# Kernel optimization log

Hardware: AMD Instinct MI355X
Metric: run time of the kernel (lower is better)

The kernel has to match this reference:

```python
import jax, jax.numpy as jnp
import numpy as np

N, A, OBS, H, E, ITERS = 2000, 16, 64, 128, 16000, 8


def _init_linear(key, din, dout):
    kw, kb = jax.random.split(key)
    s = 1.0 / np.sqrt(din)
    W = jax.random.uniform(kw, (dout, din), minval=-s, maxval=s, dtype=jnp.float32)
    b = jax.random.uniform(kb, (dout,), minval=-s, maxval=s, dtype=jnp.float32)
    return W, b


def setup_inputs() -> dict:
    key = jax.random.key(0)
    ks = jax.random.split(key, 20)
    x = jax.random.normal(ks[0], (N, OBS), dtype=jnp.float32)
    prev_action = jax.random.normal(ks[1], (N, A), dtype=jnp.float32)
    state = jax.random.normal(ks[2], (1, N, H), dtype=jnp.float32)
    # edges: unique-ish random pairs with i < j (no self loops)
    rng = np.random.default_rng(0)
    ei = rng.integers(0, N - 1, size=E)
    ej = rng.integers(ei + 1, N)
    edges = jnp.asarray(np.stack([ei, ej], axis=1), dtype=jnp.int32)
    # GRU params (torch layout: rows = [r; z; n])
    s = 1.0 / np.sqrt(H)
    gru_wih = jax.random.uniform(ks[3], (3 * H, OBS + A), minval=-s, maxval=s, dtype=jnp.float32)
    gru_whh = jax.random.uniform(ks[4], (3 * H, H), minval=-s, maxval=s, dtype=jnp.float32)
    gru_bih = jax.random.uniform(ks[5], (3 * H,), minval=-s, maxval=s, dtype=jnp.float32)
    gru_bhh = jax.random.uniform(ks[6], (3 * H,), minval=-s, maxval=s, dtype=jnp.float32)
    # utility MLP: [H, 256, 256, A]
    uW0, ub0 = _init_linear(ks[7], H, 256)
    uW1, ub1 = _init_linear(ks[8], 256, 256)
    uW2, ub2 = _init_linear(ks[9], 256, A)
    # payoff MLP: [2H, H, 256, 256, A, A*A]  (faithful to source's dim-list reuse)
    pW0, pb0 = _init_linear(ks[10], 2 * H, H)
    pW1, pb1 = _init_linear(ks[11], H, 256)
    pW2, pb2 = _init_linear(ks[12], 256, 256)
    pW3, pb3 = _init_linear(ks[13], 256, A)
    pW4, pb4 = _init_linear(ks[14], A, A * A)
    return dict(x=x, prev_action=prev_action, state=state, edges=edges,
                gru_wih=gru_wih, gru_whh=gru_whh, gru_bih=gru_bih, gru_bhh=gru_bhh,
                uW0=uW0, ub0=ub0, uW1=uW1, ub1=ub1, uW2=uW2, ub2=ub2,
                pW0=pW0, pb0=pb0, pW1=pW1, pb1=pb1, pW2=pW2, pb2=pb2,
                pW3=pW3, pb3=pb3, pW4=pW4, pb4=pb4)


def _mlp(x, params):
    n = len(params)
    for i, (W, b) in enumerate(params):
        x = x @ W.T + b
        if i < n - 1:
            x = jax.nn.relu(x)
    return x


def _gru_step(inp, h, wih, whh, bih, bhh):
    gi = inp @ wih.T + bih          # [N, 3H]
    gh = h @ whh.T + bhh            # [N, 3H]
    gir, giz, gin = jnp.split(gi, 3, axis=-1)
    ghr, ghz, ghn = jnp.split(gh, 3, axis=-1)
    r = jax.nn.sigmoid(gir + ghr)
    z = jax.nn.sigmoid(giz + ghz)
    n = jnp.tanh(gin + r * ghn)
    return (1.0 - z) * n + z * h


def _message_passing(u, p, ei, ej):
    """u: [N,A] differentiable, p: [E,A,A] differentiable.
    Messages are computed under stop_gradient (torch.no_grad in source);
    Q of the per-iteration greedy action is differentiable in u, p."""
    u_sg = jax.lax.stop_gradient(u)
    p_sg = jax.lax.stop_gradient(p)
    node_idx = jnp.arange(N)
    edge_idx = jnp.arange(E)

    def step(carry, _):
        M, q_max, opt_a = carry            # M[recv, send, A]
        S = M.sum(axis=1)                  # [N, A] total incoming per node
        base_i = u_sg[ei] + S[ei] - M[ei, ej]   # [E, A] indexed by a_i
        base_j = u_sg[ej] + S[ej] - M[ej, ei]   # [E, A] indexed by a_j
        # message i -> j: max over a_i of (p[e,ai,aj] + base_i[ai])
        msg_to_j = (p_sg + base_i[:, :, None]).max(axis=1)   # [E, A]
        msg_to_j = msg_to_j - msg_to_j.mean(axis=-1, keepdims=True)
        # message j -> i (source reduces over dim 0 = a_i; replicated faithfully)
        msg_to_i = (p_sg + base_j[:, None, :]).max(axis=1)   # [E, A]
        msg_to_i = msg_to_i - msg_to_i.mean(axis=-1, keepdims=True)
        M = M.at[ej, ei].set(msg_to_j).at[ei, ej].set(msg_to_i)
        # greedy action per node
        a_idx = jnp.argmax(u_sg + M.sum(axis=1), axis=-1)    # [N]
        q_real = u[node_idx, a_idx].sum() + p[edge_idx, a_idx[ei], a_idx[ej]].sum()
        better = q_real > q_max
        q_max = jnp.where(better, q_real, q_max)
        a_onehot = jax.nn.one_hot(a_idx, A, dtype=u.dtype)
        opt_a = jnp.where(better, a_onehot, opt_a)
        return (M, q_max, opt_a), None

    M0 = jnp.zeros((N, N, A), dtype=u.dtype)
    q0 = jnp.zeros((), dtype=u.dtype)
    a0 = jnp.zeros((N, A), dtype=u.dtype)
    (M, q_max, opt_a), _ = jax.lax.scan(step, (M0, q0, a0), None, length=ITERS)
    return opt_a, q_max


def reference(x, prev_action, state, edges,
              gru_wih, gru_whh, gru_bih, gru_bhh,
              uW0, ub0, uW1, ub1, uW2, ub2,
              pW0, pb0, pW1, pb1, pW2, pb2, pW3, pb3, pW4, pb4):
    ei, ej = edges[:, 0], edges[:, 1]
    enc_in = jnp.concatenate([x, prev_action], axis=-1)        # [N, OBS+A]
    h = _gru_step(enc_in, state[0], gru_wih, gru_whh, gru_bih, gru_bhh)  # [N, H]
    state_out = h.reshape(1, 1, N, H)
    u_params = [(uW0, ub0), (uW1, ub1), (uW2, ub2)]
    p_params = [(pW0, pb0), (pW1, pb1), (pW2, pb2), (pW3, pb3), (pW4, pb4)]
    u = _mlp(h, u_params) / N                                  # [N, A]
    s_ij = jnp.concatenate([h[ei], h[ej]], axis=-1)            # [E, 2H]
    s_ji = jnp.concatenate([h[ej], h[ei]], axis=-1)
    p_ij = _mlp(s_ij, p_params).reshape(E, A, A) / E
    p_ji = _mlp(s_ji, p_params).reshape(E, A, A) / E
    p = 0.5 * (p_ij + p_ji)                                    # [E, A, A]
    a, q_max = _message_passing(u, p, ei, ej)
    return (a, q_max, u[None], p, state_out)
```

## Files before the change

### kernel.cpp

```cpp
#include <hip/hip_runtime.h>
#include <math.h>

#define N_NODES 2000
#define NA 16
#define NOBS 64
#define NH 128
#define NE 16000
#define NITERS 8

#define WS_MSG       0
#define WS_FLAGS     300000
#define WS_Q         512000
#define WS_SBUF      512016
#define WS_AIDX      800016
#define WS_W         816016
#define WS_PT        832016
#define WS_GIT       (WS_PT + 4000000)
#define WS_GHT       (WS_GIT + 30720)
#define WS_WB        4928016
#define WS_UW0T      (WS_WB + 0)
#define WS_UWCAT     (WS_WB + 32768)
#define WS_UW1T      (WS_WB + 65536)
#define WS_UW2T      (WS_WB + 131072)
#define WS_CAB       (WS_WB + 241664)

#define F16_W1H 0
#define F16_W1L 32768
#define F16_W2H 65536
#define F16_W2L 131072
#define F16_W3H 196608
#define F16_W3L 200704
#define F16_W4H 204800
#define F16_W4L 212992

#define NBLK 500

typedef _Float16 half8 __attribute__((ext_vector_type(8)));
typedef float f32x4 __attribute__((ext_vector_type(4)));

#define AGST(p, v) __hip_atomic_store((p), (v), __ATOMIC_RELAXED, __HIP_MEMORY_SCOPE_AGENT)

__global__ __launch_bounds__(256) void setup_kernel(
    float* __restrict__ ws, const int* __restrict__ edges,
    const float* __restrict__ uW0, const float* __restrict__ uW1,
    const float* __restrict__ uW2, const float* __restrict__ pW0,
    const float* __restrict__ pW1, const float* __restrict__ pW2,
    const float* __restrict__ pW3, const float* __restrict__ pW4,
    const float* __restrict__ gwih, const float* __restrict__ gwhh)
{
    if (blockIdx.x >= 1336) {
        int e = (blockIdx.x - 1336) * 256 + threadIdx.x;
        if (e < NE) {
            int i = edges[2 * e], j = edges[2 * e + 1];
            ((int*)(ws + WS_PT))[i * N_NODES + j] = -1;
        }
        return;
    }
    int t = blockIdx.x * 256 + threadIdx.x;
    if (t >= 341904) return;
    if (t < 16) { ws[WS_Q + t] = 0.f; return; }
    t -= 16;
    if (t < 16256) { ((int*)(ws + WS_FLAGS))[t] = 0; return; }
    t -= 16256;
    if (t < 32768) {
        int o = t >> 7, k = t & 127;
        ws[WS_UW0T + k * 256 + o] = uW0[t];
        return;
    }
    t -= 32768;
    if (t < 32768) {
        int r = t >> 8, c = t & 255;
        float v = pW0[t];
        int dst = (c < 128) ? (c * 256 + r) : ((c - 128) * 256 + r + 128);
        ws[WS_UWCAT + dst] = v;
        return;
    }
    t -= 32768;
    if (t < 65536) {
        int r = t >> 8, c = t & 255;
        ws[WS_UW1T + c * 256 + r] = uW1[t];
        return;
    }
    t -= 65536;
    if (t < 4096) {
        int r = t >> 8, c = t & 255;
        ws[WS_UW2T + c * 16 + r] = uW2[t];
        return;
    }
    t -= 4096;
    if (t < 30720) {
        int g = t / 80, kk = t % 80;
        ws[WS_GIT + (kk >> 2) * 1536 + g * 4 + (kk & 3)] = gwih[t];
        return;
    }
    t -= 30720;
    if (t < 49152) {
        int g = t >> 7, kk = t & 127;
        ws[WS_GHT + (kk >> 2) * 1536 + g * 4 + (kk & 3)] = gwhh[t];
        return;
    }
    t -= 49152;
    {
        int q = t;
        _Float16* fwp = (_Float16*)ws;
        float v; int hoff, loff;
        if (q < 32768) {
            v = pW1[q]; hoff = F16_W1H + q; loff = F16_W1L + q;
        } else if (q < 98304) {
            int z = q - 32768; v = pW2[z];
            hoff = F16_W2H + z; loff = F16_W2L + z;
        } else if (q < 102400) {
            int z = q - 98304; v = pW3[z];
            hoff = F16_W3H + z; loff = F16_W3L + z;
        } else {
            int z = q - 102400; int n = z >> 5, kk = z & 31;
            v = (kk < 16) ? pW4[n * 16 + kk] : 0.f;
            hoff = F16_W4H + z; loff = F16_W4L + z;
        }
        _Float16 hv = (_Float16)v;
        fwp[hoff] = hv;
        fwp[loff] = (_Float16)(v - (float)hv);
    }
}

__device__ __forceinline__ void grid_bar(int* flags, int gval)
{
    int* gen8 = flags + NBLK * 32;
    __syncthreads();
    if (blockIdx.x == 0) {
        const int i = threadIdx.x;
        if (i >= 1 && i < NBLK) {
            while (__hip_atomic_load(&flags[i * 32], __ATOMIC_RELAXED,
                                     __HIP_MEMORY_SCOPE_AGENT) < gval)
                __builtin_amdgcn_s_sleep(2);
        }
        __syncthreads();
        if (i < 8)
            __hip_atomic_store(&gen8[i * 32], gval, __ATOMIC_RELAXED,
                               __HIP_MEMORY_SCOPE_AGENT);
    } else {
        if (threadIdx.x == 0) {
            asm volatile("s_waitcnt vmcnt(0)" ::: "memory");
            __hip_atomic_store(&flags[blockIdx.x * 32], gval, __ATOMIC_RELAXED,
                               __HIP_MEMORY_SCOPE_AGENT);
            while (__hip_atomic_load(&gen8[(blockIdx.x & 7) * 32],
                                     __ATOMIC_RELAXED,
                                     __HIP_MEMORY_SCOPE_AGENT) < gval)
                __builtin_amdgcn_s_sleep(2);
        }
        __syncthreads();
    }
}

__global__ __launch_bounds__(512, 4) void mega_kernel(
    const float* __restrict__ x, const float* __restrict__ pa,
    const float* __restrict__ st, const float* __restrict__ bih,
    const float* __restrict__ bhh, const float* __restrict__ ub0,
    const float* __restrict__ ub1, const float* __restrict__ ub2,
    const float* __restrict__ b0, const float* __restrict__ b1,
    const float* __restrict__ b2, const float* __restrict__ b3,
    const float* __restrict__ b4, const int* __restrict__ edges,
    float* __restrict__ ws, float* __restrict__ h_out,
    float* __restrict__ u_out, float* __restrict__ p_out,
    float* __restrict__ a_out, float* __restrict__ q_out)
{
    __shared__ __align__(16) _Float16 Ah[64][264];
    __shared__ __align__(16) _Float16 Al[64][264];
    __shared__ float C16[64][16];
    __shared__ int fi[64], se[64];
    __shared__ int wfl_l[32];

    const int tid  = threadIdx.x;
    const int bid  = blockIdx.x;
    const int e0   = bid * 32;
    const int wid  = tid >> 6;
    const int lane = tid & 63;
    const int lrow = lane & 15;
    const int lgrp = lane >> 4;
    const int koff = 8 * lgrp;

    float* sm = (float*)&Ah[0][0];
    int*   flags = (int*)(ws + WS_FLAGS);
    int*   owner = (int*)(ws + WS_PT);
    const _Float16* fw = (const _Float16*)ws;
    float* Sbuf = ws + WS_SBUF;
    float* q    = ws + WS_Q;
    int*   aidx = (int*)(ws + WS_AIDX);
    float* cab  = ws + WS_CAB;

    if (tid < 32) {
        int i = edges[2 * (e0 + tid)], j = edges[2 * (e0 + tid) + 1];
        fi[2 * tid] = i;     se[2 * tid] = j;
        fi[2 * tid + 1] = j; se[2 * tid + 1] = i;
    }

    {
        float* enc = sm;
        float* hp  = sm + 320;
        float* gi  = sm + 832;
        float* gh  = sm + 2368;
        float* A   = sm + 3904;
        const float* wihT = ws + WS_GIT;
        const float* whhT = ws + WS_GHT;
        const int n0 = bid * 4;

        if (tid < 320) {
            int r = tid / 80, c = tid % 80;
            enc[r * 80 + c] = (c < 64) ? x[(n0 + r) * 64 + c]
                                       : pa[(n0 + r) * 16 + (c - 64)];
        }
        {
            int r = tid >> 7, c = tid & 127;
            hp[r * 128 + c] = st[(n0 + r) * 128 + c];
        }
        __syncthreads();

        if (tid < 384) {
            const int g = tid;
            float s1[4], s2[4];
            const float bi_ = bih[g], bh_ = bhh[g];
            #pragma unroll
            for (int r = 0; r < 4; ++r) { s1[r] = bi_; s2[r] = bh_; }
            #pragma unroll 5
            for (int k4 = 0; k4 < 20; ++k4) {
                const float4 wv = *(const float4*)&wihT[k4 * 1536 + g * 4];
                #pragma unroll
                for (int r = 0; r < 4; ++r) {
                    const float4 ev = *(const float4*)&enc[r * 80 + 4 * k4];
                    s1[r] = fmaf(ev.x, wv.x, fmaf(ev.y, wv.y, fmaf(ev.z, wv.z, fmaf(ev.w, wv.w, s1[r]))));
                }
            }
            #pragma unroll 4
            for (int k4 = 0; k4 < 32; ++k4) {
                const float4 wv = *(const float4*)&whhT[k4 * 1536 + g * 4];
                #pragma unroll
                for (int r = 0; r < 4; ++r) {
                    const float4 hv = *(const float4*)&hp[r * 128 + 4 * k4];
                    s2[r] = fmaf(hv.x, wv.x, fmaf(hv.y, wv.y, fmaf(hv.z, wv.z, fmaf(hv.w, wv.w, s2[r]))));
                }
            }
            #pragma unroll
            for (int r = 0; r < 4; ++r) {
                gi[r * 384 + g] = s1[r];
                gh[r * 384 + g] = s2[r];
            }
        }
        __syncthreads();

        {
            int r = tid >> 7, c = tid & 127;
            float rr = 1.f / (1.f + expf(-(gi[r * 384 + c] + gh[r * 384 + c])));
            float zz = 1.f / (1.f + expf(-(gi[r * 384 + 128 + c] + gh[r * 384 + 128 + c])));
            float nn = tanhf(gi[r * 384 + 256 + c] + rr * gh[r * 384 + 256 + c]);
            float hv = (1.f - zz) * nn + zz * hp[r * 128 + c];
            A[r * 128 + c] = hv;
            h_out[(n0 + r) * 128 + c] = hv;
        }
        if (tid < 32) {
            int e = e0 + tid;
            atomicMax(&owner[fi[2 * tid] * N_NODES + se[2 * tid]], e);
        }
    }
    grid_bar(flags, 1);

    {
        float* A = sm + 3904;
        float* B = sm + 4416;
        const int n0 = bid * 4;
        const int o  = tid & 255;
        const int r0 = (tid >> 8) * 2;

        {
            const float* wp = ws + WS_UW0T + o;
            float a0 = ub0[o], a1 = a0;
            for (int k4 = 0; k4 < 32; ++k4) {
                float w0 = wp[(4 * k4 + 0) * 256], w1 = wp[(4 * k4 + 1) * 256];
                float w2 = wp[(4 * k4 + 2) * 256], w3 = wp[(4 * k4 + 3) * 256];
                const float4 v0 = *(const float4*)&A[r0 * 128 + 4 * k4];
                const float4 v1 = *(const float4*)&A[(r0 + 1) * 128 + 4 * k4];
                a0 = fmaf(v0.x, w0, fmaf(v0.y, w1, fmaf(v0.z, w2, fmaf(v0.w, w3, a0))));
                a1 = fmaf(v1.x, w0, fmaf(v1.y, w1, fmaf(v1.z, w2, fmaf(v1.w, w3, a1))));
            }
            B[r0 * 256 + o] = fmaxf(a0, 0.f);
            B[(r0 + 1) * 256 + o] = fmaxf(a1, 0.f);
        }
        __syncthreads();
        {
            const float* wp = ws + WS_UW1T + o;
            float a0 = ub1[o], a1 = a0;
            for (int k4 = 0; k4 < 64; ++k4) {
                float w0 = wp[(4 * k4 + 0) * 256], w1 = wp[(4 * k4 + 1) * 256];
                float w2 = wp[(4 * k4 + 2) * 256], w3 = wp[(4 * k4 + 3) * 256];
                const float4 v0 = *(const float4*)&B[r0 * 256 + 4 * k4];
                const float4 v1 = *(const float4*)&B[(r0 + 1) * 256 + 4 * k4];
                a0 = fmaf(v0.x, w0, fmaf(v0.y, w1, fmaf(v0.z, w2, fmaf(v0.w, w3, a0))));
                a1 = fmaf(v1.x, w0, fmaf(v1.y, w1, fmaf(v1.z, w2, fmaf(v1.w, w3, a1))));
            }
            __syncthreads();
            B[r0 * 256 + o] = fmaxf(a0, 0.f);
            B[(r0 + 1) * 256 + o] = fmaxf(a1, 0.f);
        }
        __syncthreads();
        if (tid < 64) {
            int r = tid >> 4, oo = tid & 15;
            const float* w2t = ws + WS_UW2T;
            float acc = ub2[oo];
            for (int k4 = 0; k4 < 64; ++k4) {
                const float4 av = *(const float4*)&B[r * 256 + 4 * k4];
                acc = fmaf(av.x, w2t[(4 * k4 + 0) * 16 + oo],
                      fmaf(av.y, w2t[(4 * k4 + 1) * 16 + oo],
                      fmaf(av.z, w2t[(4 * k4 + 2) * 16 + oo],
                      fmaf(av.w, w2t[(4 * k4 + 3) * 16 + oo], acc))));
            }
            float val = acc * (1.f / N_NODES);
            int idx = (n0 + r) * 16 + oo;
            AGST(&u_out[idx], val);
            #pragma unroll
            for (int t = 0; t < NITERS + 1; ++t) AGST(&Sbuf[t * 32000 + idx], val);
        }
        {
            const float* wp = ws + WS_UWCAT + o;
            float a0 = 0.f, a1 = 0.f;
            for (int k4 = 0; k4 < 32; ++k4) {
                float w0 = wp[(4 * k4 + 0) * 256], w1 = wp[(4 * k4 + 1) * 256];
                float w2 = wp[(4 * k4 + 2) * 256], w3 = wp[(4 * k4 + 3) * 256];
                const float4 v0 = *(const float4*)&A[r0 * 128 + 4 * k4];
                const float4 v1 = *(const float4*)&A[(r0 + 1) * 128 + 4 * k4];
                a0 = fmaf(v0.x, w0, fmaf(v0.y, w1, fmaf(v0.z, w2, fmaf(v0.w, w3, a0))));
                a1 = fmaf(v1.x, w0, fmaf(v1.y, w1, fmaf(v1.z, w2, fmaf(v1.w, w3, a1))));
            }
            AGST(&cab[(n0 + r0) * 256 + o], a0);
            AGST(&cab[(n0 + r0 + 1) * 256 + o], a1);
        }
        if (tid < 32) {
            int e = e0 + tid;
            wfl_l[tid] = (owner[fi[2 * tid] * N_NODES + se[2 * tid]] == e) ? 1 : 0;
        }
    }
    grid_bar(flags, 2);

    {
        const int cl = tid & 127;
        const int rh = tid >> 7;
        const float bb = b0[cl];
        #pragma unroll 4
        for (int r = rh * 16; r < rh * 16 + 16; ++r) {
            float v = cab[fi[r] * 256 + cl] + cab[se[r] * 256 + 128 + cl] + bb;
            v = fmaxf(v, 0.f);
            _Float16 hv = (_Float16)v;
            Ah[r][cl] = hv;
            Al[r][cl] = (_Float16)(v - (float)hv);
        }
    }
    __syncthreads();

    f32x4 acc[4][2];

    #pragma unroll
    for (int mt = 0; mt < 4; ++mt)
        #pragma unroll
        for (int nt = 0; nt < 2; ++nt) acc[mt][nt] = (f32x4){0.f, 0.f, 0.f, 0.f};
    #pragma unroll
    for (int ks = 0; ks < 4; ++ks) {
        half8 ah[4], al[4];
        #pragma unroll
        for (int mt = 0; mt < 4; ++mt) {
            ah[mt] = *(const half8*)&Ah[16 * mt + lrow][32 * ks + koff];
            al[mt] = *(const half8*)&Al[16 * mt + lrow][32 * ks + koff];
        }
        #pragma unroll
        for (int nt = 0; nt < 2; ++nt) {
            const int n = 32 * wid + 16 * nt + lrow;
            half8 bh = *(const half8*)(fw + F16_W1H + n * 128 + 32 * ks + koff);
            half8 bl = *(const half8*)(fw + F16_W1L + n * 128 + 32 * ks + koff);
            #pragma unroll
            for (int mt = 0; mt < 4; ++mt) {
                acc[mt][nt] = __builtin_amdgcn_mfma_f32_16x16x32_f16(ah[mt], bh, acc[mt][nt], 0, 0, 0);
                acc[mt][nt] = __builtin_amdgcn_mfma_f32_16x16x32_f16(ah[mt], bl, acc[mt][nt], 0, 0, 0);
                acc[mt][nt] = __builtin_amdgcn_mfma_f32_16x16x32_f16(al[mt], bh, acc[mt][nt], 0, 0, 0);
            }
        }
    }
    __syncthreads();
    #pragma unroll
    for (int nt = 0; nt < 2; ++nt) {
        const int col = 32 * wid + 16 * nt + lrow;
        const float bv = b1[col];
        #pragma unroll
        for (int mt = 0; mt < 4; ++mt) {
            #pragma unroll
            for (int r = 0; r < 4; ++r) {
                const int row = 16 * mt + 4 * lgrp + r;
                float v = fmaxf(acc[mt][nt][r] + bv, 0.f);
                _Float16 hv = (_Float16)v;
                Ah[row][col] = hv;
                Al[row][col] = (_Float16)(v - (float)hv);
            }
        }
    }
    __syncthreads();

    #pragma unroll
    for (int mt = 0; mt < 4; ++mt)
        #pragma unroll
        for (int nt = 0; nt < 2; ++nt) acc[mt][nt] = (f32x4){0.f, 0.f, 0.f, 0.f};
    for (int ks = 0; ks < 8; ++ks) {
        half8 ah[4], al[4];
        #pragma unroll
        for (int mt = 0; mt < 4; ++mt) {
            ah[mt] = *(const half8*)&Ah[16 * mt + lrow][32 * ks + koff];
            al[mt] = *(const half8*)&Al[16 * mt + lrow][32 * ks + koff];
        }
        #pragma unroll
        for (int nt = 0; nt < 2; ++nt) {
            const int n = 32 * wid + 16 * nt + lrow;
            half8 bh = *(const half8*)(fw + F16_W2H + n * 256 + 32 * ks + koff);
            half8 bl = *(const half8*)(fw + F16_W2L + n * 256 + 32 * ks + koff);
            #pragma unroll
            for (int mt = 0; mt < 4; ++mt) {
                acc[mt][nt] = __builtin_amdgcn_mfma_f32_16x16x32_f16(ah[mt], bh, acc[mt][nt], 0, 0, 0);
                acc[mt][nt] = __builtin_amdgcn_mfma_f32_16x16x32_f16(ah[mt], bl, acc[mt][nt], 0, 0, 0);
                acc[mt][nt] = __builtin_amdgcn_mfma_f32_16x16x32_f16(al[mt], bh, acc[mt][nt], 0, 0, 0);
            }
        }
    }
    __syncthreads();
    #pragma unroll
    for (int nt = 0; nt < 2; ++nt) {
        const int col = 32 * wid + 16 * nt + lrow;
        const float bv = b2[col];
        #pragma unroll
        for (int mt = 0; mt < 4; ++mt) {
            #pragma unroll
            for (int r = 0; r < 4; ++r) {
                const int row = 16 * mt + 4 * lgrp + r;
                float v = fmaxf(acc[mt][nt][r] + bv, 0.f);
                _Float16 hv = (_Float16)v;
                Ah[row][col] = hv;
                Al[row][col] = (_Float16)(v - (float)hv);
            }
        }
    }
    __syncthreads();

    if (wid < 4) {
        f32x4 acc3 = {0.f, 0.f, 0.f, 0.f};
        #pragma unroll
        for (int ks = 0; ks < 8; ++ks) {
            half8 ah = *(const half8*)&Ah[16 * wid + lrow][32 * ks + koff];
            half8 al = *(const half8*)&Al[16 * wid + lrow][32 * ks + koff];
            half8 bh = *(const half8*)(fw + F16_W3H + lrow * 256 + 32 * ks + koff);
            half8 bl = *(const half8*)(fw + F16_W3L + lrow * 256 + 32 * ks + koff);
            acc3 = __builtin_amdgcn_mfma_f32_16x16x32_f16(ah, bh, acc3, 0, 0, 0);
            acc3 = __builtin_amdgcn_mfma_f32_16x16x32_f16(ah, bl, acc3, 0, 0, 0);
            acc3 = __builtin_amdgcn_mfma_f32_16x16x32_f16(al, bh, acc3, 0, 0, 0);
        }
        const float b3v = b3[lrow];
        #pragma unroll
        for (int r = 0; r < 4; ++r)
            C16[16 * wid + 4 * lgrp + r][lrow] = fmaxf(acc3[r] + b3v, 0.f);
    }
    __syncthreads();

    float* pTl = (float*)Ah;

    {
        half8 a4h[4], a4l[4];
        #pragma unroll
        for (int mt = 0; mt < 4; ++mt) {
            half8 hh, ll;
            #pragma unroll
            for (int j = 0; j < 8; ++j) { hh[j] = (_Float16)0.f; ll[j] = (_Float16)0.f; }
            if (lgrp < 2) {
                #pragma unroll
                for (int j = 0; j < 8; ++j) {
                    float v = C16[16 * mt + lrow][8 * lgrp + j];
                    _Float16 hv = (_Float16)v;
                    hh[j] = hv;
                    ll[j] = (_Float16)(v - (float)hv);
                }
            }
            a4h[mt] = hh; a4l[mt] = ll;
        }
        #pragma unroll
        for (int nt = 0; nt < 2; ++nt) {
            const int o = 32 * wid + 16 * nt + lrow;
            const float b4v = b4[o];
            half8 bh = *(const half8*)(fw + F16_W4H + o * 32 + koff);
            half8 bl = *(const half8*)(fw + F16_W4L + o * 32 + koff);
            const int ot = (o & 15) * 16 + (o >> 4);
            #pragma unroll
            for (int mt = 0; mt < 4; ++mt) {
                f32x4 a4 = {0.f, 0.f, 0.f, 0.f};
                a4 = __builtin_amdgcn_mfma_f32_16x16x32_f16(a4h[mt], bh, a4, 0, 0, 0);
                a4 = __builtin_amdgcn_mfma_f32_16x16x32_f16(a4h[mt], bl, a4, 0, 0, 0);
                a4 = __builtin_amdgcn_mfma_f32_16x16x32_f16(a4l[mt], bh, a4, 0, 0, 0);
                const int s0 = 8 * mt + 2 * lgrp;
                float pav = (0.5f * (a4[0] + a4[1]) + b4v) * (1.f / NE);
                float pbv = (0.5f * (a4[2] + a4[3]) + b4v) * (1.f / NE);
                AGST(&p_out[(e0 + s0) * 256 + o], pav);
                AGST(&p_out[(e0 + s0 + 1) * 256 + o], pbv);
                pTl[s0 * 256 + ot] = pav;
                pTl[(s0 + 1) * 256 + ot] = pbv;
            }
        }
    }
    __syncthreads();

    const int g = tid >> 4;
    const int L = tid & 15;
    const int gi2 = fi[2 * g], gj2 = se[2 * g];
    const int wf = wfl_l[g];
    float pv[16];
    #pragma unroll
    for (int a4i = 0; a4i < 4; ++a4i) {
        float4 v = *(const float4*)&pTl[g * 256 + L * 16 + 4 * a4i];
        pv[4 * a4i + 0] = v.x; pv[4 * a4i + 1] = v.y;
        pv[4 * a4i + 2] = v.z; pv[4 * a4i + 3] = v.w;
    }
    float vmax = -INFINITY;
    #pragma unroll
    for (int a = 0; a < 16; ++a) vmax = fmaxf(vmax, pv[a]);
    float mold_ij = 0.f, mold_ji = 0.f;

    for (int t = 0; t < NITERS; ++t) {
        const float* uSo = Sbuf + t * 32000;
        float* uSn = Sbuf + (t + 1) * 32000;
        const float bi = uSo[gi2 * 16 + L] - mold_ij;
        const float bj = uSo[gj2 * 16 + L] - mold_ji;
        float mj = -INFINITY;
        #pragma unroll
        for (int a = 0; a < 16; ++a)
            mj = fmaxf(mj, pv[a] + __shfl(bi, a, 16));
        float mi = vmax + bj;
        float sj = mj, si = mi;
        #pragma unroll
        for (int off = 1; off < 16; off <<= 1) {
            sj += __shfl_xor(sj, off, 16);
            si += __shfl_xor(si, off, 16);
        }
        mj -= sj * (1.f / 16.f);
        mi -= si * (1.f / 16.f);
        mold_ji = mj;
        mold_ij = mi;
        if (wf) {
            atomicAdd(&uSn[gj2 * 16 + L], mj);
            atomicAdd(&uSn[gi2 * 16 + L], mi);
        }
        grid_bar(flags, 3 + t);
    }

    if (bid < 288) {
        const int t2 = bid / 36;
        const int r2 = (bid % 36) * 512 + tid;
        const float* Sn = Sbuf + (t2 + 1) * 32000;
        float partial = 0.f;
        if (r2 < N_NODES) {
            int n = r2;
            float bv = Sn[n * 16];
            int best = 0;
            #pragma unroll
            for (int a = 1; a < 16; ++a) {
                float v = Sn[n * 16 + a];
                if (v > bv) { bv = v; best = a; }
            }
            AGST(&aidx[t2 * N_NODES + n], best);
            partial = u_out[n * 16 + best];
        } else if (r2 < N_NODES + NE) {
            int ee = r2 - N_NODES;
            int ii = edges[2 * ee], jj = edges[2 * ee + 1];
            float bvi = Sn[ii * 16]; int ai = 0;
            #pragma unroll
            for (int a = 1; a < 16; ++a) {
                float v = Sn[ii * 16 + a];
                if (v > bvi) { bvi = v; ai = a; }
            }
            float bvj = Sn[jj * 16]; int aj = 0;
            #pragma unroll
            for (int a = 1; a < 16; ++a) {
                float v = Sn[jj * 16 + a];
                if (v > bvj) { bvj = v; aj = a; }
            }
            partial = p_out[ee * 256 + ai * 16 + aj];
        }
        #pragma unroll
        for (int off = 1; off < 64; off <<= 1)
            partial += __shfl_xor(partial, off, 64);
        if ((tid & 63) == 0) atomicAdd(&q[t2], partial);
    }
    grid_bar(flags, NITERS + 3);

    const int r = bid * 512 + tid;
    if (r < N_NODES * 16) {
        float cur = 0.f; int best_t = -1;
        #pragma unroll
        for (int t2 = 0; t2 < NITERS; ++t2) {
            float qv = q[t2];
            if (qv > cur) { cur = qv; best_t = t2; }
        }
        int n = r >> 4, c = r & 15;
        float val = 0.f;
        if (best_t >= 0 && aidx[best_t * N_NODES + n] == c) val = 1.f;
        a_out[r] = val;
        if (r == 0) q_out[0] = cur;
    }
}

extern "C" void kernel_launch(void* const* d_in, const int* in_sizes, int n_in,
                              void* d_out, int out_size, void* d_ws, size_t ws_size,
                              hipStream_t stream)
{
    (void)in_sizes; (void)n_in; (void)out_size; (void)ws_size;
    const float* x    = (const float*)d_in[0];
    const float* pa   = (const float*)d_in[1];
    const float* st   = (const float*)d_in[2];
    const int*   edges= (const int*)d_in[3];
    const float* gwih = (const float*)d_in[4];
    const float* gwhh = (const float*)d_in[5];
    const float* gbih = (const float*)d_in[6];
    const float* gbhh = (const float*)d_in[7];
    const float* uW0 = (const float*)d_in[8];  const float* ub0 = (const float*)d_in[9];
    const float* uW1 = (const float*)d_in[10]; const float* ub1 = (const float*)d_in[11];
    const float* uW2 = (const float*)d_in[12]; const float* ub2 = (const float*)d_in[13];
    const float* pW0 = (const float*)d_in[14]; const float* pb0 = (const float*)d_in[15];
    const float* pW1 = (const float*)d_in[16]; const float* pb1 = (const float*)d_in[17];
    const float* pW2 = (const float*)d_in[18]; const float* pb2 = (const float*)d_in[19];
    const float* pW3 = (const float*)d_in[20]; const float* pb3 = (const float*)d_in[21];
    const float* pW4 = (const float*)d_in[22]; const float* pb4 = (const float*)d_in[23];

    float* out   = (float*)d_out;
    float* a_out = out;
    float* q_out = out + 32000;
    float* u_out = out + 32001;
    float* p_out = out + 64001;
    float* h_out = out + 4160001;

    float* ws = (float*)d_ws;

    setup_kernel<<<1399, 256, 0, stream>>>(ws, edges, uW0, uW1, uW2,
                                           pW0, pW1, pW2, pW3, pW4, gwih, gwhh);
    mega_kernel<<<NBLK, 512, 0, stream>>>(x, pa, st, gbih, gbhh,
                                          ub0, ub1, ub2,
                                          pb0, pb1, pb2, pb3, pb4,
                                          edges, ws, h_out, u_out, p_out,
                                          a_out, q_out);
}
```

Measured before the change: 248.7 us.

## Move weight transposition from setup kernel into persistent mega kernel phase

The weight transpose and fp16 hi/lo split work moves out of the large setup kernel and into a grid-stride prologue of the persistent mega kernel. A grid barrier now follows that prologue, and the owner atomicMax runs there too. The setup kernel shrinks to a small init of flags, q and the edge table. This trades a big pre-launch kernel for in-kernel work plus a grid barrier placed before the GRU phase. The ownership check is moved before the second barrier and now sits behind a local sync.

```diff
diff --git a/kernel.cpp b/kernel.cpp
--- a/kernel.cpp
+++ b/kernel.cpp
@@ -13,7 +13,6 @@
 #define WS_Q         512000
 #define WS_SBUF      512016
 #define WS_AIDX      800016
-#define WS_W         816016
 #define WS_PT        832016
 #define WS_GIT       (WS_PT + 4000000)
 #define WS_GHT       (WS_GIT + 30720)
@@ -40,86 +39,19 @@
 
 #define AGST(p, v) __hip_atomic_store((p), (v), __ATOMIC_RELAXED, __HIP_MEMORY_SCOPE_AGENT)
 
-__global__ __launch_bounds__(256) void setup_kernel(
-    float* __restrict__ ws, const int* __restrict__ edges,
-    const float* __restrict__ uW0, const float* __restrict__ uW1,
-    const float* __restrict__ uW2, const float* __restrict__ pW0,
-    const float* __restrict__ pW1, const float* __restrict__ pW2,
-    const float* __restrict__ pW3, const float* __restrict__ pW4,
-    const float* __restrict__ gwih, const float* __restrict__ gwhh)
+__global__ __launch_bounds__(256) void init_kernel(
+    float* __restrict__ ws, const int* __restrict__ edges)
 {
-    if (blockIdx.x >= 1336) {
-        int e = (blockIdx.x - 1336) * 256 + threadIdx.x;
+    if (blockIdx.x < 64) {
+        int t = blockIdx.x * 256 + threadIdx.x;
+        if (t < 16) ws[WS_Q + t] = 0.f;
+        if (t < 16256) ((int*)(ws + WS_FLAGS))[t] = 0;
+    } else {
+        int e = (blockIdx.x - 64) * 256 + threadIdx.x;
         if (e < NE) {
             int i = edges[2 * e], j = edges[2 * e + 1];
             ((int*)(ws + WS_PT))[i * N_NODES + j] = -1;
         }
-        return;
-    }
-    int t = blockIdx.x * 256 + threadIdx.x;
-    if (t >= 341904) return;
-    if (t < 16) { ws[WS_Q + t] = 0.f; return; }
-    t -= 16;
-    if (t < 16256) { ((int*)(ws + WS_FLAGS))[t] = 0; return; }
-    t -= 16256;
-    if (t < 32768) {
-        int o = t >> 7, k = t & 127;
-        ws[WS_UW0T + k * 256 + o] = uW0[t];
-        return;
-    }
-    t -= 32768;
-    if (t < 32768) {
-        int r = t >> 8, c = t & 255;
-        float v = pW0[t];
-        int dst = (c < 128) ? (c * 256 + r) : ((c - 128) * 256 + r + 128);
-        ws[WS_UWCAT + dst] = v;
-        return;
-    }
-    t -= 32768;
-    if (t < 65536) {
-        int r = t >> 8, c = t & 255;
-        ws[WS_UW1T + c * 256 + r] = uW1[t];
-        return;
-    }
-    t -= 65536;
-    if (t < 4096) {
-        int r = t >> 8, c = t & 255;
-        ws[WS_UW2T + c * 16 + r] = uW2[t];
-        return;
-    }
-    t -= 4096;
-    if (t < 30720) {
-        int g = t / 80, kk = t % 80;
-        ws[WS_GIT + (kk >> 2) * 1536 + g * 4 + (kk & 3)] = gwih[t];
-        return;
-    }
-    t -= 30720;
-    if (t < 49152) {
-        int g = t >> 7, kk = t & 127;
-        ws[WS_GHT + (kk >> 2) * 1536 + g * 4 + (kk & 3)] = gwhh[t];
-        return;
-    }
-    t -= 49152;
-    {
-        int q = t;
-        _Float16* fwp = (_Float16*)ws;
-        float v; int hoff, loff;
-        if (q < 32768) {
-            v = pW1[q]; hoff = F16_W1H + q; loff = F16_W1L + q;
-        } else if (q < 98304) {
-            int z = q - 32768; v = pW2[z];
-            hoff = F16_W2H + z; loff = F16_W2L + z;
-        } else if (q < 102400) {
-            int z = q - 98304; v = pW3[z];
-            hoff = F16_W3H + z; loff = F16_W3L + z;
-        } else {
-            int z = q - 102400; int n = z >> 5, kk = z & 31;
-            v = (kk < 16) ? pW4[n * 16 + kk] : 0.f;
-            hoff = F16_W4H + z; loff = F16_W4L + z;
-        }
-        _Float16 hv = (_Float16)v;
-        fwp[hoff] = hv;
-        fwp[loff] = (_Float16)(v - (float)hv);
     }
 }
 
@@ -162,7 +94,12 @@
     const float* __restrict__ b4, const int* __restrict__ edges,
     float* __restrict__ ws, float* __restrict__ h_out,
     float* __restrict__ u_out, float* __restrict__ p_out,
-    float* __restrict__ a_out, float* __restrict__ q_out)
+    float* __restrict__ a_out, float* __restrict__ q_out,
+    const float* __restrict__ uW0, const float* __restrict__ uW1,
+    const float* __restrict__ uW2, const float* __restrict__ pW0,
+    const float* __restrict__ pW1, const float* __restrict__ pW2,
+    const float* __restrict__ pW3, const float* __restrict__ pW4,
+    const float* __restrict__ gwih, const float* __restrict__ gwhh)
 {
     __shared__ __align__(16) _Float16 Ah[64][264];
     __shared__ __align__(16) _Float16 Al[64][264];
@@ -193,6 +130,64 @@
         fi[2 * tid] = i;     se[2 * tid] = j;
         fi[2 * tid + 1] = j; se[2 * tid + 1] = i;
     }
+    __syncthreads();
+
+    {
+        const int gid = bid * 512 + tid;
+        for (int t = gid; t < 325632; t += NBLK * 512) {
+            int z = t;
+            if (z < 32768) {
+                int o = z >> 7, k = z & 127;
+                AGST(&ws[WS_UW0T + k * 256 + o], uW0[z]);
+            } else if ((z -= 32768) < 32768) {
+                int r = z >> 8, c = z & 255;
+                float v = pW0[z];
+                int dst = (c < 128) ? (c * 256 + r) : ((c - 128) * 256 + r + 128);
+                AGST(&ws[WS_UWCAT + dst], v);
+            } else if ((z -= 32768) < 65536) {
+                int r = z >> 8, c = z & 255;
+                AGST(&ws[WS_UW1T + c * 256 + r], uW1[z]);
+            } else if ((z -= 65536) < 4096) {
+                int r = z >> 8, c = z & 255;
+                AGST(&ws[WS_UW2T + c * 16 + r], uW2[z]);
+            } else if ((z -= 4096) < 30720) {
+                int g = z / 80, kk = z % 80;
+                AGST(&ws[WS_GIT + (kk >> 2) * 1536 + g * 4 + (kk & 3)], gwih[z]);
+            } else if ((z -= 30720) < 49152) {
+                int g = z >> 7, kk = z & 127;
+                AGST(&ws[WS_GHT + (kk >> 2) * 1536 + g * 4 + (kk & 3)], gwhh[z]);
+            } else {
+                int q2 = z - 49152;
+                float v; int hoff, loff;
+                if (q2 < 32768) {
+                    v = pW1[q2]; hoff = F16_W1H + q2; loff = F16_W1L + q2;
+                } else if (q2 < 98304) {
+                    int y = q2 - 32768; v = pW2[y];
+                    hoff = F16_W2H + y; loff = F16_W2L + y;
+                } else if (q2 < 102400) {
+                    int y = q2 - 98304; v = pW3[y];
+                    hoff = F16_W3H + y; loff = F16_W3L + y;
+                } else {
+                    int y = q2 - 102400; int n = y >> 5, kk = y & 31;
+                    v = (kk < 16) ? pW4[n * 16 + kk] : 0.f;
+                    hoff = F16_W4H + y; loff = F16_W4L + y;
+                }
+                _Float16 hv = (_Float16)v;
+                _Float16 lv = (_Float16)(v - (float)hv);
+                unsigned short hb, lb;
+                __builtin_memcpy(&hb, &hv, 2);
+                __builtin_memcpy(&lb, &lv, 2);
+                __hip_atomic_store((unsigned short*)ws + hoff, hb,
+                                   __ATOMIC_RELAXED, __HIP_MEMORY_SCOPE_AGENT);
+                __hip_atomic_store((unsigned short*)ws + loff, lb,
+                                   __ATOMIC_RELAXED, __HIP_MEMORY_SCOPE_AGENT);
+            }
+        }
+        if (tid < 32) {
+            atomicMax(&owner[fi[2 * tid] * N_NODES + se[2 * tid]], e0 + tid);
+        }
+    }
+    grid_bar(flags, 1);
 
     {
         float* enc = sm;
@@ -258,10 +253,10 @@
         }
         if (tid < 32) {
             int e = e0 + tid;
-            atomicMax(&owner[fi[2 * tid] * N_NODES + se[2 * tid]], e);
-        }
-    }
-    grid_bar(flags, 1);
+            wfl_l[tid] = (owner[fi[2 * tid] * N_NODES + se[2 * tid]] == e) ? 1 : 0;
+        }
+    }
+    __syncthreads();
 
     {
         float* A = sm + 3904;
@@ -331,10 +326,6 @@
             }
             AGST(&cab[(n0 + r0) * 256 + o], a0);
             AGST(&cab[(n0 + r0 + 1) * 256 + o], a1);
-        }
-        if (tid < 32) {
-            int e = e0 + tid;
-            wfl_l[tid] = (owner[fi[2 * tid] * N_NODES + se[2 * tid]] == e) ? 1 : 0;
         }
     }
     grid_bar(flags, 2);
@@ -637,11 +628,13 @@
 
     float* ws = (float*)d_ws;
 
-    setup_kernel<<<1399, 256, 0, stream>>>(ws, edges, uW0, uW1, uW2,
-                                           pW0, pW1, pW2, pW3, pW4, gwih, gwhh);
+    init_kernel<<<127, 256, 0, stream>>>(ws, edges);
     mega_kernel<<<NBLK, 512, 0, stream>>>(x, pa, st, gbih, gbhh,
                                           ub0, ub1, ub2,
                                           pb0, pb1, pb2, pb3, pb4,
                                           edges, ws, h_out, u_out, p_out,
-                                          a_out, q_out);
+                                          a_out, q_out,
+                                          uW0, uW1, uW2,
+                                          pW0, pW1, pW2, pW3, pW4,
+                                          gwih, gwhh);
 }
```

New measurement: 250.9 us. No clear change (+0.9%).
